# Kernel optimization log

Measured on AMD Instinct MI355X. Metric: run time of the kernel, lower is better.

The kernel has to match this reference:

```python
import jax, jax.numpy as jnp
import numpy as np

LN_EPS = 1e-5
C_HEAD = 32
N_HEAD = 4

def _layernorm(x, g, b):
    mu = jnp.mean(x, axis=-1, keepdims=True)
    var = jnp.var(x, axis=-1, keepdims=True)
    return (x - mu) * jax.lax.rsqrt(var + LN_EPS) * g + b

def setup_inputs() -> dict:
    key = jax.random.key(0)
    ks = jax.random.split(key, 5)
    B, N, c_z = 1, 256, 128
    H, c = N_HEAD, C_HEAD
    sc = lambda fan_in: 1.0 / np.sqrt(fan_in)
    return {
        "z_ij": jax.random.normal(ks[0], (B, N, N, c_z), dtype=jnp.float32),
        "ln_g": jnp.ones((c_z,), dtype=jnp.float32),
        "ln_b": jnp.zeros((c_z,), dtype=jnp.float32),
        # weights stored (in, out) = torch Linear weight transposed
        "W_qkv": jax.random.normal(ks[1], (c_z, 3 * H * c), dtype=jnp.float32) * sc(c_z),
        "W_b": jax.random.normal(ks[2], (c_z, H), dtype=jnp.float32) * sc(c_z),
        "W_g": jax.random.normal(ks[3], (c_z, H * c), dtype=jnp.float32) * sc(c_z),
        "W_o": jax.random.normal(ks[4], (H * c, c_z), dtype=jnp.float32) * sc(H * c),
    }

def reference(z_ij, ln_g, ln_b, W_qkv, W_b, W_g, W_o):
    B, N, _, c_z = z_ij.shape
    H, c = N_HEAD, C_HEAD
    z = _layernorm(z_ij, ln_g, ln_b)                      # (B,N,N,c_z)
    qkv = z @ W_qkv                                        # (B,N,N,3*H*c)
    q, k, v = (qkv[..., :H*c].reshape(B, N, N, H, c),
               qkv[..., H*c:2*H*c].reshape(B, N, N, H, c),
               qkv[..., 2*H*c:].reshape(B, N, N, H, c))
    bias = (z @ W_b).transpose(0, 3, 1, 2)                 # (B,H,j,k)
    gate = jax.nn.sigmoid(z @ W_g).reshape(B, N, N, H, c)  # (B,i,j,H,c)
    # scores[b,h,i,j,k] = (1/sqrt(c)) * q[b,i,j,h,:]\cdot k[b,i,k,h,:] + bias[b,h,j,k]
    scores = jnp.einsum('bijhc,bikhc->bhijk', q, k) / np.sqrt(c).astype(np.float32)
    scores = scores + bias[:, :, None]                     # broadcast over i
    attn = jax.nn.softmax(scores, axis=-1)                 # (B,H,i,j,k)
    o = jnp.einsum('bhijk,bikhc->bijhc', attn, v)          # (B,i,j,H,c)
    o = (gate * o).reshape(B, N, N, H * c)
    return o @ W_o                                         # (B,N,N,c_z)
```

## Files before the change

### kernel.cpp

```cpp
#include <hip/hip_runtime.h>
#include <hip/hip_bf16.h>
#include <math.h>

#define N 256
#define CZ 128
#define NH 4
#define CH 32
#define NPOS (N*N)
#define LDP 136
#define SHIFT 12.0f
#define LOG2E 1.4426950408889634f

typedef __hip_bfloat16 bf16;
typedef short bf16x4 __attribute__((ext_vector_type(4)));
typedef short bf16x8 __attribute__((ext_vector_type(8)));
typedef float f32x4 __attribute__((ext_vector_type(4)));
typedef unsigned u32x2 __attribute__((ext_vector_type(2)));

__device__ __forceinline__ float b2f(bf16 x) { return __bfloat162float(x); }
__device__ __forceinline__ bf16 f2b(float x) { return __float2bfloat16(x); }
__device__ __forceinline__ unsigned short fbits(float f) {
    bf16 h = f2b(f); unsigned short u; __builtin_memcpy(&u, &h, 2); return u;
}
__device__ __forceinline__ float s2f(short s) {
    unsigned x = ((unsigned)(unsigned short)s) << 16;
    float f; __builtin_memcpy(&f, &x, 4); return f;
}

__device__ __forceinline__ float fast_exp2(float x) { return exp2f(x); }

__device__ __forceinline__ unsigned packbf(float lo, float hi) {
    return (unsigned)fbits(lo) | ((unsigned)fbits(hi) << 16);
}

__device__ __forceinline__ u32x2 plane32_swap(unsigned a, unsigned b) {
#if __has_builtin(__builtin_amdgcn_permlane32_swap)
    return __builtin_amdgcn_permlane32_swap(a, b, false, false);
#else
    unsigned as = (unsigned)__shfl_xor((int)a, 32, 64);
    unsigned bs = (unsigned)__shfl_xor((int)b, 32, 64);
    bool up = (threadIdx.x & 32) != 0;
    u32x2 r; r.x = up ? bs : a; r.y = up ? b : as; return r;
#endif
}

__device__ __forceinline__ u32x2 plane16_swap(unsigned a, unsigned b) {
#if __has_builtin(__builtin_amdgcn_permlane16_swap)
    return __builtin_amdgcn_permlane16_swap(a, b, false, false);
#else
    unsigned as = (unsigned)__shfl_xor((int)a, 16, 64);
    unsigned bs = (unsigned)__shfl_xor((int)b, 16, 64);
    bool odd = (threadIdx.x & 16) != 0;
    u32x2 r; r.x = odd ? bs : a; r.y = odd ? b : as; return r;
#endif
}

template<typename T> __device__ __forceinline__ float ldx(const void* p, size_t i);
template<> __device__ __forceinline__ float ldx<float>(const void* p, size_t i) { return ((const float*)p)[i]; }
template<> __device__ __forceinline__ float ldx<bf16 >(const void* p, size_t i) { return b2f(((const bf16*)p)[i]); }

template<typename T> __device__ __forceinline__ void stx(void* p, size_t i, float v);
template<> __device__ __forceinline__ void stx<float>(void* p, size_t i, float v) { ((float*)p)[i] = v; }
template<> __device__ __forceinline__ void stx<bf16 >(void* p, size_t i, float v) { ((bf16*)p)[i] = f2b(v); }

template<typename T> __device__ __forceinline__ float4 ld4(const void* p, size_t i);
template<> __device__ __forceinline__ float4 ld4<float>(const void* p, size_t i) {
    return *(const float4*)((const float*)p + i);
}
template<> __device__ __forceinline__ float4 ld4<bf16>(const void* p, size_t i) {
    bf16x4 v = *(const bf16x4*)((const bf16*)p + i);
    return make_float4(s2f(v[0]), s2f(v[1]), s2f(v[2]), s2f(v[3]));
}

__device__ __forceinline__ bool input_is_f32(const void* lng) {
    return ((const unsigned*)lng)[0] == 0x3F800000u;
}

template<typename T>
__device__ void transpose_w_body(const void* Wqkv, const void* Wb, const void* Wg,
                                 const void* Wo, bf16* wtqkv, bf16* wgt, bf16* wot) {
    int idx0 = blockIdx.x*256 + threadIdx.x;
    int stride = gridDim.x*256;
    for (int idx = idx0; idx < 400*CZ; idx += stride) {
        int col = idx >> 7, ch = idx & 127;
        float v;
        if (col < 384)      v = ldx<T>(Wqkv, (size_t)ch*384 + col);
        else if (col < 388) v = ldx<T>(Wb,   (size_t)ch*NH + (col - 384));
        else                v = 0.0f;
        wtqkv[idx] = f2b(v);
    }
    for (int idx = idx0; idx < CZ*CZ; idx += stride) {
        int col = idx >> 7, ch = idx & 127;
        wgt[idx] = f2b(ldx<T>(Wg, (size_t)ch*CZ + col));
        wot[idx] = f2b(ldx<T>(Wo, (size_t)ch*CZ + col));
    }
}

__global__ __launch_bounds__(256) void transpose_w_kernel(
    const void* lng, const void* Wqkv, const void* Wb, const void* Wg, const void* Wo,
    bf16* wtqkv, bf16* wgt, bf16* wot) {
    if (input_is_f32(lng)) transpose_w_body<float>(Wqkv, Wb, Wg, Wo, wtqkv, wgt, wot);
    else                   transpose_w_body<bf16 >(Wqkv, Wb, Wg, Wo, wtqkv, wgt, wot);
}

template<typename T>
__device__ void ln_qkv_body(
    const void* z, const void* lng, const void* lnb,
    const bf16* __restrict__ wtqkv,
    bf16* zn, bf16* qo, bf16* ko, bf16* vt, float* biasF, bf16 (*zsh)[LDP])
{
    const int tid = threadIdx.x;
    const size_t base = (size_t)blockIdx.x * 128;
    const int l32 = tid & 31, rgrp = tid >> 5;

    const float4 g  = ld4<T>(lng, l32*4);
    const float4 bb = ld4<T>(lnb, l32*4);

    #pragma unroll
    for (int pass = 0; pass < 16; pass++) {
        int row = pass*8 + rgrp;
        size_t gofs = (base + row)*CZ + l32*4;
        float4 v = ld4<T>(z, gofs);
        float s1 = v.x + v.y + v.z + v.w;
        float s2 = v.x*v.x + v.y*v.y + v.z*v.z + v.w*v.w;
        #pragma unroll
        for (int off = 1; off < 32; off <<= 1) {
            s1 += __shfl_xor(s1, off, 32);
            s2 += __shfl_xor(s2, off, 32);
        }
        float mu = s1*(1.f/128.f);
        float rs = rsqrtf(s2*(1.f/128.f) - mu*mu + 1e-5f);
        bf16x4 pk;
        pk[0] = (short)fbits((v.x - mu)*rs*g.x + bb.x);
        pk[1] = (short)fbits((v.y - mu)*rs*g.y + bb.y);
        pk[2] = (short)fbits((v.z - mu)*rs*g.z + bb.z);
        pk[3] = (short)fbits((v.w - mu)*rs*g.w + bb.w);
        *(bf16x4*)&zsh[row][l32*4] = pk;
        *(bf16x4*)(zn + gofs) = pk;
    }
    __syncthreads();

    const int lane = tid & 63, wid = tid >> 6;
    const int n = lane & 15, q = lane >> 4;
    const float scale = 0.17677669529663687f * LOG2E;

    bf16x8 a[2][4];
    #pragma unroll
    for (int mt = 0; mt < 2; mt++)
        #pragma unroll
        for (int ks = 0; ks < 4; ks++)
            a[mt][ks] = *(const bf16x8*)&zsh[wid*32 + mt*16 + n][ks*32 + q*8];

    f32x4 acc[2][8];

    #pragma unroll
    for (int nt = 0; nt < 8; nt++) {
        int col = nt*16 + n;
        bf16x8 b[4];
        #pragma unroll
        for (int ks = 0; ks < 4; ks++)
            b[ks] = *(const bf16x8*)(wtqkv + (size_t)col*CZ + ks*32 + q*8);
        #pragma unroll
        for (int mt = 0; mt < 2; mt++) {
            acc[mt][nt] = (f32x4){0.f,0.f,0.f,0.f};
            #pragma unroll
            for (int ks = 0; ks < 4; ks++)
                acc[mt][nt] = __builtin_amdgcn_mfma_f32_16x16x32_bf16(a[mt][ks], b[ks], acc[mt][nt], 0, 0, 0);
        }
    }
    #pragma unroll
    for (int nt = 0; nt < 8; nt++)
        #pragma unroll
        for (int mt = 0; mt < 2; mt++) {
            size_t rowg = base + wid*32 + mt*16 + q*4;
            #pragma unroll
            for (int r = 0; r < 4; r++)
                qo[(rowg + r)*CZ + nt*16 + n] = f2b(acc[mt][nt][r]);
        }

    #pragma unroll
    for (int nt = 0; nt < 8; nt++) {
        int col = 128 + nt*16 + n;
        bf16x8 b[4];
        #pragma unroll
        for (int ks = 0; ks < 4; ks++)
            b[ks] = *(const bf16x8*)(wtqkv + (size_t)col*CZ + ks*32 + q*8);
        #pragma unroll
        for (int mt = 0; mt < 2; mt++) {
            acc[mt][nt] = (f32x4){0.f,0.f,0.f,0.f};
            #pragma unroll
            for (int ks = 0; ks < 4; ks++)
                acc[mt][nt] = __builtin_amdgcn_mfma_f32_16x16x32_bf16(a[mt][ks], b[ks], acc[mt][nt], 0, 0, 0);
        }
    }
    #pragma unroll
    for (int nt = 0; nt < 8; nt++)
        #pragma unroll
        for (int mt = 0; mt < 2; mt++) {
            size_t rowg = base + wid*32 + mt*16 + q*4;
            #pragma unroll
            for (int r = 0; r < 4; r++)
                ko[(rowg + r)*CZ + nt*16 + n] = f2b(acc[mt][nt][r]*scale);
        }

    #pragma unroll
    for (int nt = 0; nt < 8; nt++) {
        int col = 256 + nt*16 + n;
        bf16x8 b[4];
        #pragma unroll
        for (int ks = 0; ks < 4; ks++)
            b[ks] = *(const bf16x8*)(wtqkv + (size_t)col*CZ + ks*32 + q*8);
        #pragma unroll
        for (int mt = 0; mt < 2; mt++) {
            acc[mt][nt] = (f32x4){0.f,0.f,0.f,0.f};
            #pragma unroll
            for (int ks = 0; ks < 4; ks++)
                acc[mt][nt] = __builtin_amdgcn_mfma_f32_16x16x32_bf16(a[mt][ks], b[ks], acc[mt][nt], 0, 0, 0);
        }
    }
    #pragma unroll
    for (int nt = 0; nt < 8; nt++) {
        int hc = nt*16 + n;
        int hh = hc >> 5, cc = hc & 31;
        #pragma unroll
        for (int mt = 0; mt < 2; mt++) {
            size_t pos0 = base + wid*32 + mt*16 + q*4;
            int i_ = (int)(pos0 >> 8), j0 = (int)(pos0 & 255);
            bf16x4 pk;
            pk[0] = (short)fbits(acc[mt][nt][0]);
            pk[1] = (short)fbits(acc[mt][nt][1]);
            pk[2] = (short)fbits(acc[mt][nt][2]);
            pk[3] = (short)fbits(acc[mt][nt][3]);
            *(bf16x4*)(vt + (((size_t)(hh*N + i_))*CH + cc)*N + j0) = pk;
        }
    }

    {
        int col = 384 + n;
        bf16x8 b[4];
        #pragma unroll
        for (int ks = 0; ks < 4; ks++)
            b[ks] = *(const bf16x8*)(wtqkv + (size_t)col*CZ + ks*32 + q*8);
        f32x4 accb[2];
        #pragma unroll
        for (int mt = 0; mt < 2; mt++) {
            accb[mt] = (f32x4){0.f,0.f,0.f,0.f};
            #pragma unroll
            for (int ks = 0; ks < 4; ks++)
                accb[mt] = __builtin_amdgcn_mfma_f32_16x16x32_bf16(a[mt][ks], b[ks], accb[mt], 0, 0, 0);
        }
        if (n < NH) {
            int h = n;
            #pragma unroll
            for (int mt = 0; mt < 2; mt++) {
                size_t rowg = base + wid*32 + mt*16 + q*4;
                #pragma unroll
                for (int r = 0; r < 4; r++) {
                    size_t pos = rowg + r;
                    int j = (int)(pos >> 8), k = (int)(pos & 255);
                    size_t idx = ((((size_t)(h*16 + (k >> 4)))*16 + (j >> 4))*64
                                  + ((k >> 2) & 3)*16 + (j & 15))*4 + (k & 3);
                    biasF[idx] = (accb[mt][r] - SHIFT) * LOG2E;
                }
            }
        }
    }
}

__global__ __launch_bounds__(256, 2) void ln_qkv_kernel(
    const void* z, const void* lng, const void* lnb, const bf16* wtqkv,
    bf16* zn, bf16* qo, bf16* ko, bf16* vt, float* biasF)
{
    __shared__ bf16 zsh[128][LDP];
    if (input_is_f32(lng))
        ln_qkv_body<float>(z, lng, lnb, wtqkv, zn, qo, ko, vt, biasF, zsh);
    else
        ln_qkv_body<bf16 >(z, lng, lnb, wtqkv, zn, qo, ko, vt, biasF, zsh);
}

__global__ __launch_bounds__(256, 4) void attn_mfma_kernel(
    bf16* __restrict__ qws, const bf16* __restrict__ kws,
    const bf16* __restrict__ vtws, const float* __restrict__ biasF)
{
    const int h = blockIdx.x, i = blockIdx.y;
    const int lane = threadIdx.x & 63, wid = threadIdx.x >> 6;
    const int n = lane & 15, q = lane >> 4;
    const int j0w = wid * 64;

    bf16x8 bQ[4];
    #pragma unroll
    for (int jt = 0; jt < 4; jt++) {
        size_t off = ((size_t)(i*N + j0w + jt*16 + n))*CZ + h*CH + q*8;
        bQ[jt] = *(const bf16x8*)(qws + off);
    }

    f32x4 Oa[2][4];
    #pragma unroll
    for (int ct = 0; ct < 2; ct++)
        #pragma unroll
        for (int jt = 0; jt < 4; jt++) Oa[ct][jt] = (f32x4){0.f,0.f,0.f,0.f};
    float lsum[4] = {0.f, 0.f, 0.f, 0.f};

    const float* bF = biasF + (size_t)h*NPOS;

    #pragma unroll
    for (int it = 0; it < 8; it++) {
        const int k0 = it * 32;
        bf16x8 aK[2], aV[2];
        #pragma unroll
        for (int kt = 0; kt < 2; kt++) {
            size_t off = ((size_t)(i*N + k0 + kt*16 + n))*CZ + h*CH + q*8;
            aK[kt] = *(const bf16x8*)(kws + off);
        }
        #pragma unroll
        for (int ct = 0; ct < 2; ct++) {
            size_t off = (((size_t)(h*N + i))*CH + ct*16 + n)*N + k0 + q*8;
            aV[ct] = *(const bf16x8*)(vtws + off);
        }

        const int ktg0 = k0 >> 4;
        #pragma unroll
        for (int jt = 0; jt < 4; jt++) {
            unsigned S0, S1, S2, S3;
            #pragma unroll
            for (int kt = 0; kt < 2; kt++) {
                f32x4 c = *(const f32x4*)(bF
                    + ((((size_t)(ktg0 + kt))*16 + (wid*4 + jt))*64 + lane)*4);
                f32x4 s = __builtin_amdgcn_mfma_f32_16x16x32_bf16(aK[kt], bQ[jt], c, 0, 0, 0);
                float p0 = fast_exp2(s[0]), p1 = fast_exp2(s[1]);
                float p2 = fast_exp2(s[2]), p3 = fast_exp2(s[3]);
                lsum[jt] += (p0 + p1) + (p2 + p3);
                unsigned wlo = packbf(p0, p1), whi = packbf(p2, p3);
                if (kt == 0) { S0 = wlo; S1 = whi; }
                else         { S2 = wlo; S3 = whi; }
            }
            u32x2 r0 = plane32_swap(S0, S2);
            u32x2 r1 = plane32_swap(S1, S3);
            u32x2 t0 = plane16_swap(r0.x, r0.y);
            u32x2 t1 = plane16_swap(r1.x, r1.y);
            unsigned wds[4] = { t0.x, t1.x, t0.y, t1.y };
            bf16x8 bP; __builtin_memcpy(&bP, wds, 16);
            #pragma unroll
            for (int ct = 0; ct < 2; ct++)
                Oa[ct][jt] = __builtin_amdgcn_mfma_f32_16x16x32_bf16(aV[ct], bP, Oa[ct][jt], 0, 0, 0);
        }
    }

    #pragma unroll
    for (int jt = 0; jt < 4; jt++) {
        float l = lsum[jt];
        l += __shfl_xor(l, 16, 64);
        l += __shfl_xor(l, 32, 64);
        float inv = 1.0f / l;
        size_t pbase = ((size_t)(i*N + j0w + jt*16 + n))*CZ + h*CH;
        #pragma unroll
        for (int ct = 0; ct < 2; ct++)
            #pragma unroll
            for (int r = 0; r < 4; r++)
                qws[pbase + ct*16 + q*4 + r] = f2b(Oa[ct][jt][r] * inv);
    }
}

template<typename T>
__device__ void gate_out_body(
    const bf16* __restrict__ zn,
    const bf16* __restrict__ wgt, const bf16* __restrict__ wot,
    const bf16* __restrict__ ows, void* out, bf16 (*osh)[LDP])
{
    const int tid = threadIdx.x;
    const size_t base = (size_t)blockIdx.x * 64;
    const int lane = tid & 63, wid = tid >> 6;
    const int n = lane & 15, q = lane >> 4;

    bf16x8 a[4];
    #pragma unroll
    for (int ks = 0; ks < 4; ks++)
        a[ks] = *(const bf16x8*)(zn + (base + wid*16 + n)*CZ + ks*32 + q*8);

    for (int idx = tid; idx < 64*64; idx += 256) {
        int row = idx >> 6, d = idx & 63;
        ((unsigned*)&osh[row][0])[d] = ((const unsigned*)(ows + (base + row)*CZ))[d];
    }
    __syncthreads();

    float gated[8][4];
    #pragma unroll
    for (int nt = 0; nt < 8; nt++) {
        bf16x8 b[4];
        #pragma unroll
        for (int ks = 0; ks < 4; ks++)
            b[ks] = *(const bf16x8*)(wgt + (size_t)(nt*16 + n)*CZ + ks*32 + q*8);
        f32x4 acc = {0.f, 0.f, 0.f, 0.f};
        #pragma unroll
        for (int ks = 0; ks < 4; ks++)
            acc = __builtin_amdgcn_mfma_f32_16x16x32_bf16(a[ks], b[ks], acc, 0, 0, 0);
        #pragma unroll
        for (int r = 0; r < 4; r++) {
            float g = 1.0f / (1.0f + __expf(-acc[r]));
            gated[nt][r] = g * b2f(osh[wid*16 + q*4 + r][nt*16 + n]);
        }
    }
    __syncthreads();

    #pragma unroll
    for (int nt = 0; nt < 8; nt++)
        #pragma unroll
        for (int r = 0; r < 4; r++)
            osh[wid*16 + q*4 + r][nt*16 + n] = f2b(gated[nt][r]);
    __syncthreads();

    bf16x8 ga[4];
    #pragma unroll
    for (int ks = 0; ks < 4; ks++)
        ga[ks] = *(const bf16x8*)&osh[wid*16 + n][ks*32 + q*8];

    #pragma unroll
    for (int nt = 0; nt < 8; nt++) {
        bf16x8 b[4];
        #pragma unroll
        for (int ks = 0; ks < 4; ks++)
            b[ks] = *(const bf16x8*)(wot + (size_t)(nt*16 + n)*CZ + ks*32 + q*8);
        f32x4 acc = {0.f, 0.f, 0.f, 0.f};
        #pragma unroll
        for (int ks = 0; ks < 4; ks++)
            acc = __builtin_amdgcn_mfma_f32_16x16x32_bf16(ga[ks], b[ks], acc, 0, 0, 0);
        #pragma unroll
        for (int r = 0; r < 4; r++)
            stx<T>(out, (base + wid*16 + q*4 + r)*CZ + nt*16 + n, acc[r]);
    }
}

__global__ __launch_bounds__(256) void gate_out_kernel(
    const void* lng, const bf16* zn, const bf16* wgt, const bf16* wot,
    const bf16* ows, void* out)
{
    __shared__ bf16 osh[64][LDP];
    if (input_is_f32(lng))
        gate_out_body<float>(zn, wgt, wot, ows, out, osh);
    else
        gate_out_body<bf16 >(zn, wgt, wot, ows, out, osh);
}

extern "C" void kernel_launch(void* const* d_in, const int* in_sizes, int n_in,
                              void* d_out, int out_size, void* d_ws, size_t ws_size,
                              hipStream_t stream) {
    const void* z    = d_in[0];
    const void* lng  = d_in[1];
    const void* lnb  = d_in[2];
    const void* Wqkv = d_in[3];
    const void* Wb   = d_in[4];
    const void* Wg   = d_in[5];
    const void* Wo   = d_in[6];

    char* ws = (char*)d_ws;
    const size_t SZ_BF = (size_t)NPOS * CZ * sizeof(bf16);
    bf16*  qws   = (bf16*) (ws);
    bf16*  kws   = (bf16*) (ws + SZ_BF);
    bf16*  vtws  = (bf16*) (ws + 2*SZ_BF);
    bf16*  znws  = (bf16*) (ws + 3*SZ_BF);
    float* biasF = (float*)(ws + 4*SZ_BF);
    char*  wbase = ws + 4*SZ_BF + (size_t)NH*NPOS*sizeof(float);
    bf16*  wtqkv = (bf16*)(wbase);
    bf16*  wgt   = (bf16*)(wbase + (size_t)400*CZ*sizeof(bf16));
    bf16*  wot   = (bf16*)(wbase + (size_t)400*CZ*sizeof(bf16) + CZ*CZ*sizeof(bf16));

    hipLaunchKernelGGL(transpose_w_kernel, dim3(32), dim3(256), 0, stream,
                       lng, Wqkv, Wb, Wg, Wo, wtqkv, wgt, wot);
    hipLaunchKernelGGL(ln_qkv_kernel, dim3(NPOS/128), dim3(256), 0, stream,
                       z, lng, lnb, wtqkv, znws, qws, kws, vtws, biasF);
    hipLaunchKernelGGL(attn_mfma_kernel, dim3(NH, N), dim3(256), 0, stream,
                       qws, kws, vtws, biasF);
    hipLaunchKernelGGL(gate_out_kernel, dim3(NPOS/64), dim3(256), 0, stream,
                       lng, znws, wgt, wot, qws, d_out);
}
```

Baseline: 205.0 us.

## Stage projection weights through LDS with register prefetch in LN-QKV and gate-out

Weight tiles for the QKV/bias projection and for the gate and output projections are now cooperatively loaded into shared memory, with the next tile prefetched into registers while the current one is in use. Each wave's B-operand fragments then come from LDS instead of repeated scattered global/L2 reads. Barriers are replaced by a waitcnt-plus-s_barrier helper, and ln_qkv's occupancy hint is raised from 2 to 4 blocks. In exchange there are more barriers, extra register pressure from the prefetch buffers, and more LDS in gate_out, which can lower occupancy.

```diff
diff --git a/kernel.cpp b/kernel.cpp
--- a/kernel.cpp
+++ b/kernel.cpp
@@ -28,6 +28,12 @@
 }
 
 __device__ __forceinline__ float fast_exp2(float x) { return exp2f(x); }
+
+__device__ __forceinline__ void lgkm_barrier() {
+    asm volatile("s_waitcnt lgkmcnt(0)" ::: "memory");
+    __builtin_amdgcn_s_barrier();
+    asm volatile("" ::: "memory");
+}
 
 __device__ __forceinline__ unsigned packbf(float lo, float hi) {
     return (unsigned)fbits(lo) | ((unsigned)fbits(hi) << 16);
@@ -107,11 +113,18 @@
 __device__ void ln_qkv_body(
     const void* z, const void* lng, const void* lnb,
     const bf16* __restrict__ wtqkv,
-    bf16* zn, bf16* qo, bf16* ko, bf16* vt, float* biasF, bf16 (*zsh)[LDP])
+    bf16* zn, bf16* qo, bf16* ko, bf16* vt, float* biasF,
+    bf16 (*sh)[LDP])
 {
     const int tid = threadIdx.x;
     const size_t base = (size_t)blockIdx.x * 128;
     const int l32 = tid & 31, rgrp = tid >> 5;
+    const int wrow = tid >> 4, wcol = tid & 15;
+
+    bf16x8 wpre[8];
+    #pragma unroll
+    for (int p = 0; p < 8; p++)
+        wpre[p] = *(const bf16x8*)(wtqkv + (size_t)(p*16 + wrow)*CZ + wcol*8);
 
     const float4 g  = ld4<T>(lng, l32*4);
     const float4 bb = ld4<T>(lnb, l32*4);
@@ -135,10 +148,10 @@
         pk[1] = (short)fbits((v.y - mu)*rs*g.y + bb.y);
         pk[2] = (short)fbits((v.z - mu)*rs*g.z + bb.z);
         pk[3] = (short)fbits((v.w - mu)*rs*g.w + bb.w);
-        *(bf16x4*)&zsh[row][l32*4] = pk;
+        *(bf16x4*)&sh[row][l32*4] = pk;
         *(bf16x4*)(zn + gofs) = pk;
     }
-    __syncthreads();
+    lgkm_barrier();
 
     const int lane = tid & 63, wid = tid >> 6;
     const int n = lane & 15, q = lane >> 4;
@@ -149,17 +162,25 @@
     for (int mt = 0; mt < 2; mt++)
         #pragma unroll
         for (int ks = 0; ks < 4; ks++)
-            a[mt][ks] = *(const bf16x8*)&zsh[wid*32 + mt*16 + n][ks*32 + q*8];
+            a[mt][ks] = *(const bf16x8*)&sh[wid*32 + mt*16 + n][ks*32 + q*8];
+    lgkm_barrier();
+
+    #pragma unroll
+    for (int p = 0; p < 8; p++)
+        *(bf16x8*)&sh[p*16 + wrow][wcol*8] = wpre[p];
+    #pragma unroll
+    for (int p = 0; p < 8; p++)
+        wpre[p] = *(const bf16x8*)(wtqkv + (size_t)(128 + p*16 + wrow)*CZ + wcol*8);
+    lgkm_barrier();
 
     f32x4 acc[2][8];
 
     #pragma unroll
     for (int nt = 0; nt < 8; nt++) {
-        int col = nt*16 + n;
         bf16x8 b[4];
         #pragma unroll
         for (int ks = 0; ks < 4; ks++)
-            b[ks] = *(const bf16x8*)(wtqkv + (size_t)col*CZ + ks*32 + q*8);
+            b[ks] = *(const bf16x8*)&sh[nt*16 + n][ks*32 + q*8];
         #pragma unroll
         for (int mt = 0; mt < 2; mt++) {
             acc[mt][nt] = (f32x4){0.f,0.f,0.f,0.f};
@@ -177,14 +198,25 @@
             for (int r = 0; r < 4; r++)
                 qo[(rowg + r)*CZ + nt*16 + n] = f2b(acc[mt][nt][r]);
         }
+    lgkm_barrier();
+
+    #pragma unroll
+    for (int p = 0; p < 8; p++)
+        *(bf16x8*)&sh[p*16 + wrow][wcol*8] = wpre[p];
+    #pragma unroll
+    for (int p = 0; p < 8; p++)
+        wpre[p] = *(const bf16x8*)(wtqkv + (size_t)(256 + p*16 + wrow)*CZ + wcol*8);
+    bf16x8 vtail;
+    if (tid < 64)
+        vtail = *(const bf16x8*)(wtqkv + (size_t)(384 + (tid >> 4))*CZ + (tid & 15)*8);
+    lgkm_barrier();
 
     #pragma unroll
     for (int nt = 0; nt < 8; nt++) {
-        int col = 128 + nt*16 + n;
         bf16x8 b[4];
         #pragma unroll
         for (int ks = 0; ks < 4; ks++)
-            b[ks] = *(const bf16x8*)(wtqkv + (size_t)col*CZ + ks*32 + q*8);
+            b[ks] = *(const bf16x8*)&sh[nt*16 + n][ks*32 + q*8];
         #pragma unroll
         for (int mt = 0; mt < 2; mt++) {
             acc[mt][nt] = (f32x4){0.f,0.f,0.f,0.f};
@@ -202,14 +234,21 @@
             for (int r = 0; r < 4; r++)
                 ko[(rowg + r)*CZ + nt*16 + n] = f2b(acc[mt][nt][r]*scale);
         }
+    lgkm_barrier();
+
+    #pragma unroll
+    for (int p = 0; p < 8; p++)
+        *(bf16x8*)&sh[p*16 + wrow][wcol*8] = wpre[p];
+    if (tid < 64)
+        *(bf16x8*)&sh[128 + (tid >> 4)][(tid & 15)*8] = vtail;
+    lgkm_barrier();
 
     #pragma unroll
     for (int nt = 0; nt < 8; nt++) {
-        int col = 256 + nt*16 + n;
         bf16x8 b[4];
         #pragma unroll
         for (int ks = 0; ks < 4; ks++)
-            b[ks] = *(const bf16x8*)(wtqkv + (size_t)col*CZ + ks*32 + q*8);
+            b[ks] = *(const bf16x8*)&sh[nt*16 + n][ks*32 + q*8];
         #pragma unroll
         for (int mt = 0; mt < 2; mt++) {
             acc[mt][nt] = (f32x4){0.f,0.f,0.f,0.f};
@@ -236,11 +275,10 @@
     }
 
     {
-        int col = 384 + n;
         bf16x8 b[4];
         #pragma unroll
         for (int ks = 0; ks < 4; ks++)
-            b[ks] = *(const bf16x8*)(wtqkv + (size_t)col*CZ + ks*32 + q*8);
+            b[ks] = *(const bf16x8*)&sh[128 + n][ks*32 + q*8];
         f32x4 accb[2];
         #pragma unroll
         for (int mt = 0; mt < 2; mt++) {
@@ -267,15 +305,15 @@
     }
 }
 
-__global__ __launch_bounds__(256, 2) void ln_qkv_kernel(
+__global__ __launch_bounds__(256, 4) void ln_qkv_kernel(
     const void* z, const void* lng, const void* lnb, const bf16* wtqkv,
     bf16* zn, bf16* qo, bf16* ko, bf16* vt, float* biasF)
 {
-    __shared__ bf16 zsh[128][LDP];
+    __shared__ bf16 sh[132][LDP];
     if (input_is_f32(lng))
-        ln_qkv_body<float>(z, lng, lnb, wtqkv, zn, qo, ko, vt, biasF, zsh);
+        ln_qkv_body<float>(z, lng, lnb, wtqkv, zn, qo, ko, vt, biasF, sh);
     else
-        ln_qkv_body<bf16 >(z, lng, lnb, wtqkv, zn, qo, ko, vt, biasF, zsh);
+        ln_qkv_body<bf16 >(z, lng, lnb, wtqkv, zn, qo, ko, vt, biasF, sh);
 }
 
 __global__ __launch_bounds__(256, 4) void attn_mfma_kernel(
@@ -365,12 +403,19 @@
 __device__ void gate_out_body(
     const bf16* __restrict__ zn,
     const bf16* __restrict__ wgt, const bf16* __restrict__ wot,
-    const bf16* __restrict__ ows, void* out, bf16 (*osh)[LDP])
+    const bf16* __restrict__ ows, void* out,
+    bf16 (*osh)[LDP], bf16 (*wsh)[LDP])
 {
     const int tid = threadIdx.x;
     const size_t base = (size_t)blockIdx.x * 64;
     const int lane = tid & 63, wid = tid >> 6;
     const int n = lane & 15, q = lane >> 4;
+    const int wrow = tid >> 4, wcol = tid & 15;
+
+    bf16x8 wopre[8];
+    #pragma unroll
+    for (int p = 0; p < 8; p++)
+        wopre[p] = *(const bf16x8*)(wot + (size_t)(p*16 + wrow)*CZ + wcol*8);
 
     bf16x8 a[4];
     #pragma unroll
@@ -381,7 +426,10 @@
         int row = idx >> 6, d = idx & 63;
         ((unsigned*)&osh[row][0])[d] = ((const unsigned*)(ows + (base + row)*CZ))[d];
     }
-    __syncthreads();
+    #pragma unroll
+    for (int p = 0; p < 8; p++)
+        *(bf16x8*)&wsh[p*16 + wrow][wcol*8] = *(const bf16x8*)(wgt + (size_t)(p*16 + wrow)*CZ + wcol*8);
+    lgkm_barrier();
 
     float gated[8][4];
     #pragma unroll
@@ -389,7 +437,7 @@
         bf16x8 b[4];
         #pragma unroll
         for (int ks = 0; ks < 4; ks++)
-            b[ks] = *(const bf16x8*)(wgt + (size_t)(nt*16 + n)*CZ + ks*32 + q*8);
+            b[ks] = *(const bf16x8*)&wsh[nt*16 + n][ks*32 + q*8];
         f32x4 acc = {0.f, 0.f, 0.f, 0.f};
         #pragma unroll
         for (int ks = 0; ks < 4; ks++)
@@ -400,14 +448,17 @@
             gated[nt][r] = g * b2f(osh[wid*16 + q*4 + r][nt*16 + n]);
         }
     }
-    __syncthreads();
-
+    lgkm_barrier();
+
+    #pragma unroll
+    for (int p = 0; p < 8; p++)
+        *(bf16x8*)&wsh[p*16 + wrow][wcol*8] = wopre[p];
     #pragma unroll
     for (int nt = 0; nt < 8; nt++)
         #pragma unroll
         for (int r = 0; r < 4; r++)
             osh[wid*16 + q*4 + r][nt*16 + n] = f2b(gated[nt][r]);
-    __syncthreads();
+    lgkm_barrier();
 
     bf16x8 ga[4];
     #pragma unroll
@@ -419,7 +470,7 @@
         bf16x8 b[4];
         #pragma unroll
         for (int ks = 0; ks < 4; ks++)
-            b[ks] = *(const bf16x8*)(wot + (size_t)(nt*16 + n)*CZ + ks*32 + q*8);
+            b[ks] = *(const bf16x8*)&wsh[nt*16 + n][ks*32 + q*8];
         f32x4 acc = {0.f, 0.f, 0.f, 0.f};
         #pragma unroll
         for (int ks = 0; ks < 4; ks++)
@@ -435,10 +486,11 @@
     const bf16* ows, void* out)
 {
     __shared__ bf16 osh[64][LDP];
+    __shared__ bf16 wsh[128][LDP];
     if (input_is_f32(lng))
-        gate_out_body<float>(zn, wgt, wot, ows, out, osh);
+        gate_out_body<float>(zn, wgt, wot, ows, out, osh, wsh);
     else
-        gate_out_body<bf16 >(zn, wgt, wot, ows, out, osh);
+        gate_out_body<bf16 >(zn, wgt, wot, ows, out, osh, wsh);
 }
 
 extern "C" void kernel_launch(void* const* d_in, const int* in_sizes, int n_in,
```

Result: faster. 191.4 us (-6.6%).
